# Kernel optimization log

Measured on AMD Instinct MI355X. Metric: run time of the kernel, lower is better.

Reference implementation:

```python
import jax, jax.numpy as jnp
import numpy as np

N_NODES = 50000
N_EDGES = 600000
D = 128        # input_dim == hidden_dim
OUT = 2        # output_dim
N_LAYERS = 6


def setup_inputs() -> dict:
    key = jax.random.key(0)
    ks = jax.random.split(key, 6)
    scale = 1.0 / np.sqrt(D)
    x = jax.random.normal(ks[0], (N_NODES, D), jnp.float32)
    edge_index = jax.random.randint(ks[1], (2, N_EDGES), 0, N_NODES)
    Wl = jax.random.normal(ks[2], (N_LAYERS, D, D), jnp.float32) * scale  # neighbor (lin_l) weights
    Wr = jax.random.normal(ks[3], (N_LAYERS, D, D), jnp.float32) * scale  # root (lin_r) weights
    bl = jnp.zeros((N_LAYERS, D), jnp.float32)                            # lin_l bias
    fc_W = jax.random.normal(ks[4], (D, OUT), jnp.float32) * scale
    fc_b = jnp.zeros((OUT,), jnp.float32)
    return {"x": x, "edge_index": edge_index, "Wl": Wl, "Wr": Wr, "bl": bl,
            "fc_W": fc_W, "fc_b": fc_b}


def _sage_conv(h, src, dst, deg_inv, Wl_i, Wr_i, bl_i):
    # mean aggregation over incoming edges: gather -> scatter-add -> normalize
    agg = jax.ops.segment_sum(h[src], dst, num_segments=h.shape[0]) * deg_inv  # [N, D]
    return agg @ Wl_i + h @ Wr_i + bl_i


def reference(x, edge_index, Wl, Wr, bl, fc_W, fc_b):
    src, dst = edge_index[0], edge_index[1]
    deg = jax.ops.segment_sum(jnp.ones(src.shape, x.dtype), dst, num_segments=x.shape[0])
    deg_inv = (1.0 / jnp.maximum(deg, 1.0))[:, None]  # [N, 1]
    h = x
    # ReLU follows every SAGEConv: inner act of each GraphSAGE block + explicit F.relu after each block
    for i in range(N_LAYERS):
        h = _sage_conv(h, src, dst, deg_inv, Wl[i], Wr[i], bl[i])
        h = jax.nn.relu(h)
    return h @ fc_W + fc_b  # [N, OUT]
```

## Files before the change

### kernel.cpp

```cpp
#include <hip/hip_runtime.h>
#include <hip/hip_bf16.h>

#define N_NODES 50000
#define N_EDGES 600000
#define DD 128
#define N_LAYERS 6
#define SCAN_BLOCKS 196
#define N_CHUNKS 3125

typedef __attribute__((ext_vector_type(8))) short bf16x8;
typedef __attribute__((ext_vector_type(4))) float floatx4;

__device__ __forceinline__ void ldsdma16(const void* g, void* l) {
    __builtin_amdgcn_global_load_lds(
        (const __attribute__((address_space(1))) char*)g,
        (__attribute__((address_space(3))) char*)l, 16, 0, 0);
}

__device__ __forceinline__ unsigned short f2b(float f) {
    unsigned u = __float_as_uint(f);
    unsigned r = (u + 0x7FFFu + ((u >> 16) & 1u)) >> 16;
    return (unsigned short)r;
}


__global__ void zero_counts(int* __restrict__ deg, int* __restrict__ cursor) {
    int i = blockIdx.x * blockDim.x + threadIdx.x;
    if (i < N_NODES) { deg[i] = 0; cursor[i] = 0; }
}

__global__ void count_deg(const int* __restrict__ dst, int* __restrict__ deg) {
    int e = blockIdx.x * blockDim.x + threadIdx.x;
    if (e < N_EDGES) atomicAdd(&deg[dst[e]], 1);
}

__global__ void block_sums(const int* __restrict__ deg, int* __restrict__ bsum) {
    __shared__ int s[256];
    int tid = threadIdx.x;
    int i = blockIdx.x * 256 + tid;
    int v = (i < N_NODES) ? deg[i] : 0;
    s[tid] = v;
    __syncthreads();
    #pragma unroll
    for (int off = 128; off > 0; off >>= 1) {
        if (tid < off) s[tid] += s[tid + off];
        __syncthreads();
    }
    if (tid == 0) bsum[blockIdx.x] = s[0];
}

__global__ void scan_bsums(int* __restrict__ bsum, int* __restrict__ offsets) {
    __shared__ int s[256];
    int tid = threadIdx.x;
    int v = (tid < SCAN_BLOCKS) ? bsum[tid] : 0;
    s[tid] = v;
    __syncthreads();
    for (int off = 1; off < 256; off <<= 1) {
        int t = (tid >= off) ? s[tid - off] : 0;
        __syncthreads();
        s[tid] += t;
        __syncthreads();
    }
    if (tid < SCAN_BLOCKS) bsum[tid] = s[tid] - v;
    if (tid == 0) offsets[N_NODES] = N_EDGES;
}

__global__ void write_offsets(const int* __restrict__ deg, const int* __restrict__ bsum,
                              int* __restrict__ offsets, float* __restrict__ deg_inv) {
    __shared__ int s[256];
    int tid = threadIdx.x;
    int i = blockIdx.x * 256 + tid;
    int v = (i < N_NODES) ? deg[i] : 0;
    s[tid] = v;
    __syncthreads();
    for (int off = 1; off < 256; off <<= 1) {
        int t = (tid >= off) ? s[tid - off] : 0;
        __syncthreads();
        s[tid] += t;
        __syncthreads();
    }
    if (i < N_NODES) {
        offsets[i] = bsum[blockIdx.x] + s[tid] - v;
        deg_inv[i] = 1.0f / (float)(v > 1 ? v : 1);
    }
}

__global__ void fill_csr(const int* __restrict__ src, const int* __restrict__ dst,
                         const int* __restrict__ offsets, int* __restrict__ cursor,
                         int* __restrict__ csr_src) {
    int e = blockIdx.x * blockDim.x + threadIdx.x;
    if (e < N_EDGES) {
        int d = dst[e];
        int p = atomicAdd(&cursor[d], 1);
        csr_src[offsets[d] + p] = src[e];
    }
}


__global__ void x_to_bf16(const float* __restrict__ x, unsigned short* __restrict__ hx) {
    int idx = blockIdx.x * blockDim.x + threadIdx.x;
    int b = idx * 4;
    float4 v = *(const float4*)(x + b);
    ushort4 o;
    o.x = f2b(v.x); o.y = f2b(v.y); o.z = f2b(v.z); o.w = f2b(v.w);
    *(ushort4*)(hx + b) = o;
}

__global__ void prep_weights(const float* __restrict__ Wl, const float* __restrict__ Wr,
                             unsigned short* __restrict__ WT2) {
    int idx = blockIdx.x * blockDim.x + threadIdx.x;
    int l   = idx >> 15;
    int rem = idx & 32767;
    int n   = rem >> 8;
    int k2  = rem & 255;
    const float* W = (k2 < 128 ? Wl : Wr) + (size_t)l * DD * DD + (size_t)(k2 & 127) * DD + n;
    WT2[idx] = f2b(*W);
}


__global__ void aggregate(const unsigned short* __restrict__ hin, const int* __restrict__ offsets,
                          const int* __restrict__ csr_src, const float* __restrict__ deg_inv,
                          unsigned short* __restrict__ agg) {
    int wid  = threadIdx.x >> 6;
    int lane = threadIdx.x & 63;
    int grp  = lane >> 4;
    int l16  = lane & 15;
    int node = blockIdx.x * 4 + wid;
    if (node >= N_NODES) return;
    int s = offsets[node], e = offsets[node + 1];

    float a0=0,a1=0,a2=0,a3=0,a4=0,a5=0,a6=0,a7=0;
    for (int j = s + grp; j < e; j += 4) {
        int src = csr_src[j];
        uint4 v = *(const uint4*)(hin + (size_t)src * DD + l16 * 8);
        a0 += __uint_as_float(v.x << 16); a1 += __uint_as_float(v.x & 0xFFFF0000u);
        a2 += __uint_as_float(v.y << 16); a3 += __uint_as_float(v.y & 0xFFFF0000u);
        a4 += __uint_as_float(v.z << 16); a5 += __uint_as_float(v.z & 0xFFFF0000u);
        a6 += __uint_as_float(v.w << 16); a7 += __uint_as_float(v.w & 0xFFFF0000u);
    }
    a0 += __shfl_xor(a0, 16, 64); a1 += __shfl_xor(a1, 16, 64);
    a2 += __shfl_xor(a2, 16, 64); a3 += __shfl_xor(a3, 16, 64);
    a4 += __shfl_xor(a4, 16, 64); a5 += __shfl_xor(a5, 16, 64);
    a6 += __shfl_xor(a6, 16, 64); a7 += __shfl_xor(a7, 16, 64);
    a0 += __shfl_xor(a0, 32, 64); a1 += __shfl_xor(a1, 32, 64);
    a2 += __shfl_xor(a2, 32, 64); a3 += __shfl_xor(a3, 32, 64);
    a4 += __shfl_xor(a4, 32, 64); a5 += __shfl_xor(a5, 32, 64);
    a6 += __shfl_xor(a6, 32, 64); a7 += __shfl_xor(a7, 32, 64);

    if (grp == 0) {
        float di = deg_inv[node];
        uint4 o;
        o.x = (unsigned)f2b(a0 * di) | ((unsigned)f2b(a1 * di) << 16);
        o.y = (unsigned)f2b(a2 * di) | ((unsigned)f2b(a3 * di) << 16);
        o.z = (unsigned)f2b(a4 * di) | ((unsigned)f2b(a5 * di) << 16);
        o.w = (unsigned)f2b(a6 * di) | ((unsigned)f2b(a7 * di) << 16);
        *(uint4*)(agg + (size_t)node * DD + l16 * 8) = o;
    }
}


__launch_bounds__(512, 2)
__global__ void gemm_resW(const unsigned short* __restrict__ Agg,
                          const unsigned short* __restrict__ H,
                          const unsigned short* __restrict__ WT2,
                          const float* __restrict__ bias,
                          unsigned short* __restrict__ Cout) {
    __shared__ __align__(16) unsigned short sW[128 * 256];
    __shared__ __align__(16) unsigned short sA[8][4096];

    int tid  = threadIdx.x;
    int wid  = tid >> 6, lane = tid & 63;
    int l15  = lane & 15, q = lane >> 4;

    for (int t = tid; t < 4096; t += 512) {
        int col = t >> 5, c = t & 31;
        uint4 v = *(const uint4*)(WT2 + (size_t)col * 256 + c * 8);
        *(uint4*)(sW + ((size_t)col * 32 + (c ^ (col & 7))) * 8) = v;
    }
    __syncthreads();

    float bcol[8];
    #pragma unroll
    for (int j = 0; j < 8; ++j) bcol[j] = bias[j * 16 + l15];

    unsigned short* myA = &sA[wid][0];

    for (int chunk = blockIdx.x * 8 + wid; chunk < N_CHUNKS; chunk += 2048) {
        int row0 = chunk * 16;
        #pragma unroll
        for (int i = 0; i < 4; ++i) {
            int r  = i * 4 + q;
            int cg = l15 ^ (r & 7);
            ldsdma16(Agg + (size_t)(row0 + r) * DD + cg * 8, myA + (size_t)i * 512 + lane * 8);
        }
        #pragma unroll
        for (int i = 0; i < 4; ++i) {
            int r  = i * 4 + q;
            int cg = l15 ^ (r & 7);
            ldsdma16(H + (size_t)(row0 + r) * DD + cg * 8, myA + 2048 + (size_t)i * 512 + lane * 8);
        }
        __builtin_amdgcn_s_waitcnt(0);

        floatx4 acc[8];
        #pragma unroll
        for (int j = 0; j < 8; ++j) acc[j] = (floatx4){0.f, 0.f, 0.f, 0.f};

        #pragma unroll
        for (int s = 0; s < 8; ++s) {
            int cglob = s * 4 + q;
            int reg   = cglob >> 4;
            int cin   = cglob & 15;
            bf16x8 aF = *(const bf16x8*)(myA + (size_t)reg * 2048 +
                                         ((size_t)l15 * 16 + (cin ^ (l15 & 7))) * 8);
            #pragma unroll
            for (int j = 0; j < 8; ++j) {
                int col = j * 16 + l15;
                bf16x8 bF = *(const bf16x8*)(sW + ((size_t)col * 32 + (cglob ^ (col & 7))) * 8);
                acc[j] = __builtin_amdgcn_mfma_f32_16x16x32_bf16(aF, bF, acc[j], 0, 0, 0);
            }
        }

        #pragma unroll
        for (int r = 0; r < 4; ++r) {
            int row = row0 + q * 4 + r;
            #pragma unroll
            for (int j = 0; j < 8; ++j) {
                float v = acc[j][r] + bcol[j];
                Cout[(size_t)row * DD + j * 16 + l15] = f2b(fmaxf(v, 0.f));
            }
        }
    }
}


__global__ void fc_kernel(const unsigned short* __restrict__ h, const float* __restrict__ fcW,
                          const float* __restrict__ fcb, float* __restrict__ out) {
    int n = blockIdx.x * blockDim.x + threadIdx.x;
    if (n >= N_NODES) return;
    const unsigned* hr = (const unsigned*)(h + (size_t)n * DD);
    float s0 = fcb[0], s1 = fcb[1];
    #pragma unroll 8
    for (int k = 0; k < 64; ++k) {
        unsigned v = hr[k];
        float h0 = __uint_as_float(v << 16);
        float h1 = __uint_as_float(v & 0xFFFF0000u);
        s0 += h0 * fcW[(2 * k) * 2]     + h1 * fcW[(2 * k + 1) * 2];
        s1 += h0 * fcW[(2 * k) * 2 + 1] + h1 * fcW[(2 * k + 1) * 2 + 1];
    }
    out[n * 2] = s0; out[n * 2 + 1] = s1;
}


extern "C" void kernel_launch(void* const* d_in, const int* in_sizes, int n_in,
                              void* d_out, int out_size, void* d_ws, size_t ws_size,
                              hipStream_t stream) {
    const float* x    = (const float*)d_in[0];
    const int*   ei   = (const int*)d_in[1];
    const float* Wl   = (const float*)d_in[2];
    const float* Wr   = (const float*)d_in[3];
    const float* bl   = (const float*)d_in[4];
    const float* fcW  = (const float*)d_in[5];
    const float* fcb  = (const float*)d_in[6];
    float* out = (float*)d_out;

    const int* srcIdx = ei;
    const int* dstIdx = ei + N_EDGES;

    char* ws = (char*)d_ws;
    size_t off = 0;
    auto bump = [&](size_t bytes) { char* p = ws + off; off = (off + bytes + 255) & ~(size_t)255; return p; };
    int*   deg     = (int*)  bump(N_NODES * 4);
    int*   cursor  = (int*)  bump(N_NODES * 4);
    int*   offsets = (int*)  bump((N_NODES + 1) * 4);
    int*   bsum    = (int*)  bump(SCAN_BLOCKS * 4);
    float* deg_inv = (float*)bump(N_NODES * 4);
    int*   csr     = (int*)  bump(N_EDGES * 4);
    unsigned short* hx   = (unsigned short*)bump((size_t)N_NODES * DD * 2);
    unsigned short* hb0  = (unsigned short*)bump((size_t)N_NODES * DD * 2);
    unsigned short* hb1  = (unsigned short*)bump((size_t)N_NODES * DD * 2);
    unsigned short* agg  = (unsigned short*)bump((size_t)N_NODES * DD * 2);
    unsigned short* WT2  = (unsigned short*)bump((size_t)N_LAYERS * 128 * 256 * 2);
    (void)ws_size;

    zero_counts<<<(N_NODES + 255) / 256, 256, 0, stream>>>(deg, cursor);
    count_deg<<<(N_EDGES + 255) / 256, 256, 0, stream>>>(dstIdx, deg);
    block_sums<<<SCAN_BLOCKS, 256, 0, stream>>>(deg, bsum);
    scan_bsums<<<1, 256, 0, stream>>>(bsum, offsets);
    write_offsets<<<SCAN_BLOCKS, 256, 0, stream>>>(deg, bsum, offsets, deg_inv);
    fill_csr<<<(N_EDGES + 255) / 256, 256, 0, stream>>>(srcIdx, dstIdx, offsets, cursor, csr);
    x_to_bf16<<<(N_NODES * DD / 4 + 255) / 256, 256, 0, stream>>>(x, hx);
    prep_weights<<<(N_LAYERS * 128 * 256 + 255) / 256, 256, 0, stream>>>(Wl, Wr, WT2);

    const unsigned short* hin = hx;
    unsigned short* hbuf[2] = { hb0, hb1 };
    for (int l = 0; l < N_LAYERS; ++l) {
        aggregate<<<(N_NODES + 3) / 4, 256, 0, stream>>>(hin, offsets, csr, deg_inv, agg);
        unsigned short* hout = hbuf[l & 1];
        gemm_resW<<<256, 512, 0, stream>>>(
            agg, hin, WT2 + (size_t)l * 128 * 256, bl + (size_t)l * DD, hout);
        hin = hout;
    }
    fc_kernel<<<(N_NODES + 255) / 256, 256, 0, stream>>>(hin, fcW, fcb, out);
}
```

Baseline: 401.7 us.

## Replace LDS-staged persistent GEMM with direct global-load one-wave-per-tile GEMM

Rewrites the per-layer dense transform so that each wave handles one 16-row tile and loads its A rows and the weight fragments directly from global memory into registers for the MFMAs. The LDS staging of the full 128x256 weight matrix and of the A/H tiles via LDS DMA is removed, along with the persistent grid-stride loop. This cuts the per-block weight staging and synchronisation cost and raises occupancy, since the kernel uses no shared memory and launches one wave per tile. In exchange, weights are re-read from global memory or cache by every wave, and the A and weight loads are narrower and less coalesced.

```diff
diff --git a/kernel.cpp b/kernel.cpp
--- a/kernel.cpp
+++ b/kernel.cpp
@@ -10,12 +10,6 @@
 
 typedef __attribute__((ext_vector_type(8))) short bf16x8;
 typedef __attribute__((ext_vector_type(4))) float floatx4;
-
-__device__ __forceinline__ void ldsdma16(const void* g, void* l) {
-    __builtin_amdgcn_global_load_lds(
-        (const __attribute__((address_space(1))) char*)g,
-        (__attribute__((address_space(3))) char*)l, 16, 0, 0);
-}
 
 __device__ __forceinline__ unsigned short f2b(float f) {
     unsigned u = __float_as_uint(f);
@@ -159,75 +153,57 @@
 }
 
 
-__launch_bounds__(512, 2)
-__global__ void gemm_resW(const unsigned short* __restrict__ Agg,
-                          const unsigned short* __restrict__ H,
-                          const unsigned short* __restrict__ WT2,
-                          const float* __restrict__ bias,
-                          unsigned short* __restrict__ Cout) {
-    __shared__ __align__(16) unsigned short sW[128 * 256];
-    __shared__ __align__(16) unsigned short sA[8][4096];
-
-    int tid  = threadIdx.x;
-    int wid  = tid >> 6, lane = tid & 63;
-    int l15  = lane & 15, q = lane >> 4;
-
-    for (int t = tid; t < 4096; t += 512) {
-        int col = t >> 5, c = t & 31;
-        uint4 v = *(const uint4*)(WT2 + (size_t)col * 256 + c * 8);
-        *(uint4*)(sW + ((size_t)col * 32 + (c ^ (col & 7))) * 8) = v;
-    }
-    __syncthreads();
+__global__ void gemm_direct(const unsigned short* __restrict__ Agg,
+                            const unsigned short* __restrict__ H,
+                            const unsigned short* __restrict__ WT2,
+                            const float* __restrict__ bias,
+                            unsigned short* __restrict__ Cout) {
+    int gwave = (blockIdx.x * blockDim.x + threadIdx.x) >> 6;
+    int lane  = threadIdx.x & 63;
+    int l15   = lane & 15, q = lane >> 4;
+    if (gwave >= N_CHUNKS) return;
+    int row0 = gwave * 16;
+    int grow = row0 + l15;
+
+    const unsigned short* Arow = Agg + (size_t)grow * DD;
+    const unsigned short* Hrow = H   + (size_t)grow * DD;
 
     float bcol[8];
     #pragma unroll
     for (int j = 0; j < 8; ++j) bcol[j] = bias[j * 16 + l15];
 
-    unsigned short* myA = &sA[wid][0];
-
-    for (int chunk = blockIdx.x * 8 + wid; chunk < N_CHUNKS; chunk += 2048) {
-        int row0 = chunk * 16;
+    floatx4 acc[8];
+    #pragma unroll
+    for (int j = 0; j < 8; ++j) acc[j] = (floatx4){0.f, 0.f, 0.f, 0.f};
+
+    #pragma unroll 2
+    for (int s = 0; s < 4; ++s) {
+        bf16x8 aF = *(const bf16x8*)(Arow + s * 32 + q * 8);
         #pragma unroll
-        for (int i = 0; i < 4; ++i) {
-            int r  = i * 4 + q;
-            int cg = l15 ^ (r & 7);
-            ldsdma16(Agg + (size_t)(row0 + r) * DD + cg * 8, myA + (size_t)i * 512 + lane * 8);
+        for (int j = 0; j < 8; ++j) {
+            int col = j * 16 + l15;
+            bf16x8 bF = *(const bf16x8*)(WT2 + (size_t)col * 256 + s * 32 + q * 8);
+            acc[j] = __builtin_amdgcn_mfma_f32_16x16x32_bf16(aF, bF, acc[j], 0, 0, 0);
         }
+    }
+    #pragma unroll 2
+    for (int s = 0; s < 4; ++s) {
+        bf16x8 aF = *(const bf16x8*)(Hrow + s * 32 + q * 8);
         #pragma unroll
-        for (int i = 0; i < 4; ++i) {
-            int r  = i * 4 + q;
-            int cg = l15 ^ (r & 7);
-            ldsdma16(H + (size_t)(row0 + r) * DD + cg * 8, myA + 2048 + (size_t)i * 512 + lane * 8);
+        for (int j = 0; j < 8; ++j) {
+            int col = j * 16 + l15;
+            bf16x8 bF = *(const bf16x8*)(WT2 + (size_t)col * 256 + 128 + s * 32 + q * 8);
+            acc[j] = __builtin_amdgcn_mfma_f32_16x16x32_bf16(aF, bF, acc[j], 0, 0, 0);
         }
-        __builtin_amdgcn_s_waitcnt(0);
-
-        floatx4 acc[8];
+    }
+
+    #pragma unroll
+    for (int r = 0; r < 4; ++r) {
+        int row = row0 + q * 4 + r;
         #pragma unroll
-        for (int j = 0; j < 8; ++j) acc[j] = (floatx4){0.f, 0.f, 0.f, 0.f};
-
-        #pragma unroll
-        for (int s = 0; s < 8; ++s) {
-            int cglob = s * 4 + q;
-            int reg   = cglob >> 4;
-            int cin   = cglob & 15;
-            bf16x8 aF = *(const bf16x8*)(myA + (size_t)reg * 2048 +
-                                         ((size_t)l15 * 16 + (cin ^ (l15 & 7))) * 8);
-            #pragma unroll
-            for (int j = 0; j < 8; ++j) {
-                int col = j * 16 + l15;
-                bf16x8 bF = *(const bf16x8*)(sW + ((size_t)col * 32 + (cglob ^ (col & 7))) * 8);
-                acc[j] = __builtin_amdgcn_mfma_f32_16x16x32_bf16(aF, bF, acc[j], 0, 0, 0);
-            }
-        }
-
-        #pragma unroll
-        for (int r = 0; r < 4; ++r) {
-            int row = row0 + q * 4 + r;
-            #pragma unroll
-            for (int j = 0; j < 8; ++j) {
-                float v = acc[j][r] + bcol[j];
-                Cout[(size_t)row * DD + j * 16 + l15] = f2b(fmaxf(v, 0.f));
-            }
+        for (int j = 0; j < 8; ++j) {
+            float v = acc[j][r] + bcol[j];
+            Cout[(size_t)row * DD + j * 16 + l15] = f2b(fmaxf(v, 0.f));
         }
     }
 }
@@ -296,7 +272,7 @@
     for (int l = 0; l < N_LAYERS; ++l) {
         aggregate<<<(N_NODES + 3) / 4, 256, 0, stream>>>(hin, offsets, csr, deg_inv, agg);
         unsigned short* hout = hbuf[l & 1];
-        gemm_resW<<<256, 512, 0, stream>>>(
+        gemm_direct<<<(N_CHUNKS * 64 + 255) / 256, 256, 0, stream>>>(
             agg, hin, WT2 + (size_t)l * 128 * 256, bl + (size_t)l * DD, hout);
         hin = hout;
     }
```

Measured after the change: 545.0 us. 35.7% more time.
